# Optimization experiments

Hardware: AMD Instinct MI355X
Metric: run time of the kernel (lower is better)

## Reference

```python
import jax, jax.numpy as jnp
import numpy as np

PRIME = 2147483647  # 2^31 - 1, MinHash modulus
GAMMA = 0.3
NUM_HEADS = 8


def minhash_sketch(ids, a, b):
    # ids: (B, L, S) int64 atom ids; a,b: (K,) hash coefficients
    # h[b,l,s,k] = (a[k]*id + b[k]) mod PRIME ; signature = min over the set axis S
    h = (ids[..., None] * a + b) % PRIME          # (B, L, S, K)
    return h.min(axis=2)                          # (B, L, K)


def jaccard_from_signatures(sig_q, sig_k):
    # sig_q: (B, Lq, K), sig_k: (B, Lk, K) -> (B, Lq, Lk) fraction of matching slots.
    # Scan over the K hash slots to avoid materializing a (B,Lq,Lk,K) tensor.
    B, Lq, K = sig_q.shape
    Lk = sig_k.shape[1]

    def step(acc, cols):
        qc, kc = cols                              # (B,Lq), (B,Lk)
        return acc + (qc[:, :, None] == kc[:, None, :]).astype(jnp.float32), None

    init = jnp.zeros((B, Lq, Lk), jnp.float32)
    xs = (jnp.moveaxis(sig_q, -1, 0), jnp.moveaxis(sig_k, -1, 0))
    acc, _ = jax.lax.scan(step, init, xs)
    return acc / K


def symdiff_from_jaccard(jacc, size_q, size_k):
    # |A ∩ B| = J/(1+J) * (|A|+|B|)  =>  |A Δ B| = (|A|+|B|) * (1-J)/(1+J)
    tot = size_q[:, :, None] + size_k[:, None, :]   # (B, Lq, Lk)
    return tot * (1.0 - jacc) / (1.0 + jacc)


def setup_inputs() -> dict:
    key = jax.random.key(0)
    ks = jax.random.split(key, 12)
    B, Lq, Lk, E, S, K, V = 4, 1024, 1024, 512, 8, 128, 32000
    w = lambda k: (jax.random.normal(k, (E, E), jnp.float32) * 0.02)
    return {
        "query": jax.random.normal(ks[0], (B, Lq, E), jnp.float32),
        "key": jax.random.normal(ks[1], (B, Lk, E), jnp.float32),
        "value": jax.random.normal(ks[2], (B, Lk, E), jnp.float32),
        "token_sets_q": jax.random.randint(ks[3], (B, Lq, S), 0, V).astype(jnp.int64),
        "token_sets_k": jax.random.randint(ks[4], (B, Lk, S), 0, V).astype(jnp.int64),
        "hash_a": jax.random.randint(ks[5], (K,), 1, PRIME - 1).astype(jnp.int64),
        "hash_b": jax.random.randint(ks[6], (K,), 0, PRIME - 1).astype(jnp.int64),
        "Wq": w(ks[7]), "bq": jnp.zeros((E,), jnp.float32),
        "Wk": w(ks[8]), "bk": jnp.zeros((E,), jnp.float32),
        "Wv": w(ks[9]), "bv": jnp.zeros((E,), jnp.float32),
        "Wo": w(ks[10]), "bo": jnp.zeros((E,), jnp.float32),
    }


def reference(query, key, value, token_sets_q, token_sets_k, hash_a, hash_b,
              Wq, bq, Wk, bk, Wv, bv, Wo, bo):
    B, Lq, E = query.shape
    Lk = key.shape[1]
    H = NUM_HEADS
    d = E // H

    # in-projections (torch Linear: x @ W^T + b); q,k are computed but the
    # attention scores come solely from the token-set kernel (gating disabled)
    q = query @ Wq.T + bq
    k = key @ Wk.T + bk
    v = (value @ Wv.T + bv).reshape(B, Lk, H, d).transpose(0, 2, 1, 3)  # (B,H,Lk,d)

    # MinHash sketches of per-token atom sets -> estimated Jaccard -> Δ-RBF score
    sig_q = minhash_sketch(token_sets_q, hash_a, hash_b)   # (B,Lq,K)
    sig_k = minhash_sketch(token_sets_k, hash_a, hash_b)   # (B,Lk,K)
    jacc = jaccard_from_signatures(sig_q, sig_k)           # (B,Lq,Lk)

    S = token_sets_q.shape[-1]
    size_q = jnp.full((B, Lq), S, jnp.float32)             # uniform CSR offsets -> |set| = S
    size_k = jnp.full((B, Lk), S, jnp.float32)
    delta = symdiff_from_jaccard(jacc, size_q, size_k)
    scores = jnp.exp(-GAMMA * delta)                       # (B,Lq,Lk), shared by all heads

    attn = jax.nn.softmax(scores, axis=-1)                 # no masks, no causal, dropout=0
    ctx = jnp.einsum('bqk,bhkd->bqhd', attn, v).reshape(B, Lq, E)
    return ctx @ Wo.T + bo
```

## Files before the change

kernel.cpp:

```cpp
#include <hip/hip_runtime.h>
#include <hip/hip_bf16.h>
#include <stdint.h>

#define PRIME 2147483647u
#define GAMMA 0.3f
#define K_HASH 128
#define S_SET 8
#define NB 4
#define LQ 1024
#define LK 1024
#define EDIM 512

typedef unsigned short ushort_t;
typedef __attribute__((ext_vector_type(8))) short short8;
typedef __attribute__((ext_vector_type(4))) float f32x4;

static __device__ __forceinline__ unsigned short f2bf(float f) {
    unsigned u = __builtin_bit_cast(unsigned, f);
    u += 0x7FFFu + ((u >> 16) & 1u);
    return (unsigned short)(u >> 16);
}

static __device__ __forceinline__ void glds16(const void* g, void* l) {
    __builtin_amdgcn_global_load_lds(
        (const __attribute__((address_space(1))) unsigned int*)g,
        (__attribute__((address_space(3))) unsigned int*)l, 16, 0, 0);
}

#define SWZ(r) ((((r) >> 2) & 3) ^ ((r) & 3))

static __device__ __forceinline__ unsigned nm2(unsigned acc, unsigned a,
                                               unsigned b, unsigned ones) {
    unsigned x = a ^ b, t;
    asm("v_pk_min_u16 %0, %1, %2" : "=v"(t) : "v"(x), "v"(ones));
    return acc + t;
}
static __device__ __forceinline__ unsigned nm8(unsigned acc, int4 q, int4 k,
                                               unsigned ones) {
    acc = nm2(acc, (unsigned)q.x, (unsigned)k.x, ones);
    acc = nm2(acc, (unsigned)q.y, (unsigned)k.y, ones);
    acc = nm2(acc, (unsigned)q.z, (unsigned)k.z, ones);
    acc = nm2(acc, (unsigned)q.w, (unsigned)k.w, ones);
    return acc;
}

#define CVT_N0 (NB * LK * EDIM)
#define CVT_N1 (EDIM * EDIM)
#define CVT_N2 (EDIM * EDIM)
#define CVT_BLOCKS ((CVT_N0 + CVT_N1 + CVT_N2) / (256 * 8))
#define SIG_BLOCKS (NB * (LQ + LK) / 2)

__global__ __launch_bounds__(256) void prep_kernel(
        const float* __restrict__ v, const float* __restrict__ wv,
        const float* __restrict__ wo,
        ushort_t* __restrict__ vb, ushort_t* __restrict__ wvb,
        ushort_t* __restrict__ wob,
        const int* __restrict__ ts_q, const int* __restrict__ ts_k,
        const int* __restrict__ ha, const int* __restrict__ hb,
        ushort_t* __restrict__ sig_q, ushort_t* __restrict__ sig_k,
        float* __restrict__ rs) {
    int blk = blockIdx.x;
    if (blk < CVT_BLOCKS) {
        size_t i = ((size_t)blk * 256 + threadIdx.x) * 8;
        const float* src; ushort_t* dst; size_t off;
        if (i < CVT_N0)                { src = v;  dst = vb;  off = i; }
        else if (i < CVT_N0 + CVT_N1)  { src = wv; dst = wvb; off = i - CVT_N0; }
        else                           { src = wo; dst = wob; off = i - CVT_N0 - CVT_N1; }
        float4 a = *(const float4*)(src + off);
        float4 b = *(const float4*)(src + off + 4);
        ushort4 o0, o1;
        o0.x = f2bf(a.x); o0.y = f2bf(a.y); o0.z = f2bf(a.z); o0.w = f2bf(a.w);
        o1.x = f2bf(b.x); o1.y = f2bf(b.y); o1.z = f2bf(b.z); o1.w = f2bf(b.w);
        *(ushort4*)(dst + off)     = o0;
        *(ushort4*)(dst + off + 4) = o1;
        return;
    }
    int sb = blk - CVT_BLOCKS;
    if (sb < 16) rs[sb * 256 + threadIdx.x] = 0.f;
    int half = threadIdx.x >> 7, k = threadIdx.x & 127;
    int row = sb * 2 + half;
    const int* ts = (row < NB * LQ) ? ts_q : ts_k;
    ushort_t* sig = (row < NB * LQ) ? sig_q : sig_k;
    int idx = row & (NB * LQ - 1);
    unsigned long long a  = (unsigned)ha[k];
    unsigned long long bb = (unsigned)hb[k];
    __shared__ int ids[2][S_SET];
    if (k < S_SET) ids[half][k] = ts[idx * S_SET + k];
    __syncthreads();
    unsigned mn = 0xFFFFFFFFu;
    #pragma unroll
    for (int s = 0; s < S_SET; s++) {
        unsigned long long x = a * (unsigned long long)(unsigned)ids[half][s] + bb;
        x = (x & PRIME) + (x >> 31);
        x = (x & PRIME) + (x >> 31);
        unsigned r = (unsigned)x;
        if (r >= PRIME) r -= PRIME;
        mn = (r < mn) ? r : mn;
    }
    sig[idx * K_HASH + k] = (ushort_t)mn;
}

__global__ __launch_bounds__(256) void jaccard_kernel(
        const ushort_t* __restrict__ sig_q, const ushort_t* __restrict__ sig_k,
        ushort_t* __restrict__ P, float* __restrict__ rs) {
    __shared__ int Qs[64 * 36];
    __shared__ int Ks[64 * 36];
    __shared__ float lut[K_HASH + 1];
    int tid = threadIdx.x;
    if (tid <= K_HASH) {
        float r = (float)(K_HASH - tid) / (float)(K_HASH + tid);
        lut[tid] = expf(expf(-GAMMA * (2.0f * S_SET) * r));
    }
    int b = blockIdx.z;
    int q0 = blockIdx.y * 64, j0 = blockIdx.x * 64;
    const int4* gq = (const int4*)(sig_q + ((size_t)b * LQ + q0) * K_HASH);
    const int4* gk = (const int4*)(sig_k + ((size_t)b * LK + j0) * K_HASH);
    int tx = tid & 15, ty = tid >> 4;
    unsigned ones = 0x00010001u;
    unsigned acc[4][4] = {};
    int sr = tid >> 2, sg0 = (tid & 3) * 2;
    #pragma unroll 1
    for (int h = 0; h < 2; h++) {
        __syncthreads();
        #pragma unroll
        for (int u = 0; u < 2; u++) {
            int g = sg0 + u;
            *(int4*)&Qs[sr * 36 + ((g ^ (sr >> 2)) & 7) * 4] = gq[sr * 16 + h * 8 + g];
            *(int4*)&Ks[sr * 36 + ((g ^ (sr >> 2)) & 7) * 4] = gk[sr * 16 + h * 8 + g];
        }
        __syncthreads();
        #pragma unroll
        for (int g = 0; g < 8; g++) {
            int qx = ((g ^ ty) & 7) * 4, kx = ((g ^ tx) & 7) * 4;
            int4 qv[4], kv[4];
            #pragma unroll
            for (int i = 0; i < 4; i++)
                qv[i] = *(const int4*)&Qs[(ty * 4 + i) * 36 + qx];
            #pragma unroll
            for (int j = 0; j < 4; j++)
                kv[j] = *(const int4*)&Ks[(tx * 4 + j) * 36 + kx];
            #pragma unroll
            for (int i = 0; i < 4; i++)
                #pragma unroll
                for (int j = 0; j < 4; j++)
                    acc[i][j] = nm8(acc[i][j], qv[i], kv[j], ones);
        }
    }
    ushort_t* Pb = P + (size_t)b * LQ * LK;
    float fsum[4];
    #pragma unroll
    for (int i = 0; i < 4; i++) {
        ushort4 o;
        unsigned n0_ = (acc[i][0] & 0xFFFFu) + (acc[i][0] >> 16);
        unsigned n1_ = (acc[i][1] & 0xFFFFu) + (acc[i][1] >> 16);
        unsigned n2_ = (acc[i][2] & 0xFFFFu) + (acc[i][2] >> 16);
        unsigned n3_ = (acc[i][3] & 0xFFFFu) + (acc[i][3] >> 16);
        float p0 = lut[K_HASH - n0_], p1 = lut[K_HASH - n1_];
        float p2 = lut[K_HASH - n2_], p3 = lut[K_HASH - n3_];
        fsum[i] = (p0 + p1) + (p2 + p3);
        o.x = f2bf(p0); o.y = f2bf(p1); o.z = f2bf(p2); o.w = f2bf(p3);
        int row = q0 + ty * 4 + i;
        *(ushort4*)&Pb[(size_t)row * LK + j0 + tx * 4] = o;
    }
    __syncthreads();
    float* fs = (float*)&Qs[0];
    #pragma unroll
    for (int i = 0; i < 4; i++) fs[(ty * 4 + i) * 16 + tx] = fsum[i];
    __syncthreads();
    if (tid < 64) {
        float s = 0.f;
        #pragma unroll
        for (int t = 0; t < 16; t++) s += fs[tid * 16 + t];
        atomicAdd(&rs[(size_t)b * LQ + q0 + tid], s);
    }
}

#define EPI_ROWBIAS  0
#define EPI_ROWDIV   1
#define EPI_COLBIAS  2

template<int OUTF32, int MODE>
__global__ __launch_bounds__(256) void btgemm_kernel(
        const ushort_t* __restrict__ A, const ushort_t* __restrict__ B,
        void* __restrict__ C,
        const float* __restrict__ bias, const float* __restrict__ scale,
        int lda, int ldb, int ldc, int Kd,
        long long sA, long long sB, long long sC, long long sS) {
    __shared__ ushort_t As[2][64 * 32];
    __shared__ ushort_t Bs[2][64 * 32];
    int z = blockIdx.z;
    int m0 = blockIdx.y * 64, n0 = blockIdx.x * 64;
    int tid = threadIdx.x;
    int w = tid >> 6, lane = tid & 63;
    int wm = (w & 1) * 32, wn = (w >> 1) * 32;
    int mrow = lane & 15, kg = lane >> 4;

    int r = tid >> 2, c = (tid & 3) ^ SWZ(r);
    const ushort_t* pa = A + (size_t)z * sA + (size_t)(m0 + r) * lda + c * 8;
    const ushort_t* pb = B + (size_t)z * sB + (size_t)(n0 + r) * ldb + c * 8;

    int aoff[2], boff[2];
    #pragma unroll
    for (int s = 0; s < 2; s++) {
        int Ra = wm + s * 16 + mrow;
        aoff[s] = Ra * 32 + (kg ^ SWZ(Ra)) * 8;
        int Rb = wn + s * 16 + mrow;
        boff[s] = Rb * 32 + (kg ^ SWZ(Rb)) * 8;
    }

    f32x4 acc[2][2] = {};
    int nK = Kd >> 5;
    glds16(pa, &As[0][tid * 8]);
    glds16(pb, &Bs[0][tid * 8]);
    for (int i = 0; i < nK; i++) {
        __syncthreads();
        int cur = i & 1, nxt = cur ^ 1;
        if (i + 1 < nK) {
            int k0 = (i + 1) << 5;
            glds16(pa + k0, &As[nxt][tid * 8]);
            glds16(pb + k0, &Bs[nxt][tid * 8]);
        }
        short8 af[2], bh[2];
        #pragma unroll
        for (int s = 0; s < 2; s++) {
            af[s] = *(const short8*)&As[cur][aoff[s]];
            bh[s] = *(const short8*)&Bs[cur][boff[s]];
        }
        #pragma unroll
        for (int ii = 0; ii < 2; ii++)
            #pragma unroll
            for (int jj = 0; jj < 2; jj++)
                acc[ii][jj] = __builtin_amdgcn_mfma_f32_16x16x32_bf16(
                                  af[ii], bh[jj], acc[ii][jj], 0, 0, 0);
    }

    const float* sc = scale + (size_t)z * sS;
    int col = lane & 15, rbase = (lane >> 4) * 4;
    #pragma unroll
    for (int ii = 0; ii < 2; ii++) {
        #pragma unroll
        for (int jj = 0; jj < 2; jj++) {
            #pragma unroll
            for (int rr = 0; rr < 4; rr++) {
                int gm = m0 + wm + ii * 16 + rbase + rr;
                int gn = n0 + wn + jj * 16 + col;
                float v = acc[ii][jj][rr];
                if (MODE == EPI_ROWBIAS)     v += bias[gm];
                else if (MODE == EPI_ROWDIV) v /= sc[gm];
                else                         v += bias[gn];
                size_t cix = (size_t)z * sC + (size_t)gm * ldc + gn;
                if (OUTF32) ((float*)C)[cix] = v;
                else        ((ushort_t*)C)[cix] = f2bf(v);
            }
        }
    }
}

extern "C" void kernel_launch(void* const* d_in, const int* in_sizes, int n_in,
                              void* d_out, int out_size, void* d_ws, size_t ws_size,
                              hipStream_t stream) {
    const float* value = (const float*)d_in[2];
    const int* tsq = (const int*)d_in[3];
    const int* tsk = (const int*)d_in[4];
    const int* ha  = (const int*)d_in[5];
    const int* hb  = (const int*)d_in[6];
    const float* Wv = (const float*)d_in[11];
    const float* bv = (const float*)d_in[12];
    const float* Wo = (const float*)d_in[13];
    const float* bo = (const float*)d_in[14];
    float* out = (float*)d_out;

    char* ws = (char*)d_ws;
    ushort_t* sigq   = (ushort_t*)(ws);
    ushort_t* sigk   = (ushort_t*)(ws + (1ull << 20));
    ushort_t* P      = (ushort_t*)(ws + (4ull << 20));
    float* rs        = (float*)(ws + (12ull << 20));
    ushort_t* Vt     = (ushort_t*)(ws + (12ull << 20) + (1ull << 16));
    ushort_t* ctx    = (ushort_t*)(ws + (17ull << 20));
    ushort_t* Vb     = (ushort_t*)(ws + (21ull << 20));
    ushort_t* Wvb    = (ushort_t*)(ws + (25ull << 20));
    ushort_t* Wob    = (ushort_t*)(ws + (25ull << 20) + (512ull << 10));

    prep_kernel<<<CVT_BLOCKS + SIG_BLOCKS, 256, 0, stream>>>(
        value, Wv, Wo, Vb, Wvb, Wob, tsq, tsk, ha, hb, sigq, sigk, rs);

    jaccard_kernel<<<dim3(LK / 64, LQ / 64, NB), 256, 0, stream>>>(sigq, sigk, P, rs);

    btgemm_kernel<0, EPI_ROWBIAS><<<dim3(4096 / 64, 512 / 64, 1), 256, 0, stream>>>(
        Wvb, Vb, Vt, bv, rs ,
        EDIM, EDIM, NB * LK, EDIM, 0LL, 0LL, 0LL, 0LL);

    btgemm_kernel<0, EPI_ROWDIV><<<dim3(EDIM / 64, LQ / 64, NB), 256, 0, stream>>>(
        P, Vt, ctx, bv , rs,
        LK, NB * LK, EDIM, LK,
        (long long)LQ * LK, (long long)LK, (long long)LQ * EDIM, (long long)LQ);

    btgemm_kernel<1, EPI_COLBIAS><<<dim3(EDIM / 64, NB * LQ / 64, 1), 256, 0, stream>>>(
        ctx, Wob, out, bo, rs ,
        EDIM, EDIM, EDIM, EDIM, 0LL, 0LL, 0LL, 0LL);
}
```

Baseline: 154.8 us.

## Merge Jaccard and V-projection GEMM into one launch, enlarge Jaccard tile

Fuses the Jaccard score kernel and the V in-projection GEMM into a single launch, with odd blocks doing GEMM tiles and even blocks doing Jaccard tiles. Both share shared memory through a union. The Jaccard tile grows from 64x64 to 128x64 query-by-key, so each thread accumulates 8x4 outputs and the loaded K signatures get more reuse. The aim is to remove one launch and let the two independent stages overlap on the GPU, at the cost of more registers and shared memory per block, plus a stray no-op shared-memory write left in the load loop.

```diff
diff --git a/kernel.cpp b/kernel.cpp
--- a/kernel.cpp
+++ b/kernel.cpp
@@ -42,6 +42,83 @@
     acc = nm2(acc, (unsigned)q.z, (unsigned)k.z, ones);
     acc = nm2(acc, (unsigned)q.w, (unsigned)k.w, ones);
     return acc;
+}
+
+#define EPI_ROWBIAS  0
+#define EPI_ROWDIV   1
+#define EPI_COLBIAS  2
+
+template<int OUTF32, int MODE>
+static __device__ void gemm64_dev(
+        const ushort_t* __restrict__ A, const ushort_t* __restrict__ B,
+        void* __restrict__ C,
+        const float* __restrict__ bias, const float* __restrict__ scale,
+        int lda, int ldb, int ldc, int Kd, int m0, int n0,
+        ushort_t* AsBase, ushort_t* BsBase, int tid) {
+    ushort_t (*As)[64 * 32] = (ushort_t (*)[64 * 32])AsBase;
+    ushort_t (*Bs)[64 * 32] = (ushort_t (*)[64 * 32])BsBase;
+    int w = tid >> 6, lane = tid & 63;
+    int wm = (w & 1) * 32, wn = (w >> 1) * 32;
+    int mrow = lane & 15, kg = lane >> 4;
+
+    int r = tid >> 2, c = (tid & 3) ^ SWZ(r);
+    const ushort_t* pa = A + (size_t)(m0 + r) * lda + c * 8;
+    const ushort_t* pb = B + (size_t)(n0 + r) * ldb + c * 8;
+
+    int aoff[2], boff[2];
+    #pragma unroll
+    for (int s = 0; s < 2; s++) {
+        int Ra = wm + s * 16 + mrow;
+        aoff[s] = Ra * 32 + (kg ^ SWZ(Ra)) * 8;
+        int Rb = wn + s * 16 + mrow;
+        boff[s] = Rb * 32 + (kg ^ SWZ(Rb)) * 8;
+    }
+
+    f32x4 acc[2][2] = {};
+    int nK = Kd >> 5;
+    glds16(pa, &As[0][tid * 8]);
+    glds16(pb, &Bs[0][tid * 8]);
+    for (int i = 0; i < nK; i++) {
+        __syncthreads();
+        int cur = i & 1, nxt = cur ^ 1;
+        if (i + 1 < nK) {
+            int k0 = (i + 1) << 5;
+            glds16(pa + k0, &As[nxt][tid * 8]);
+            glds16(pb + k0, &Bs[nxt][tid * 8]);
+        }
+        short8 af[2], bh[2];
+        #pragma unroll
+        for (int s = 0; s < 2; s++) {
+            af[s] = *(const short8*)&As[cur][aoff[s]];
+            bh[s] = *(const short8*)&Bs[cur][boff[s]];
+        }
+        #pragma unroll
+        for (int ii = 0; ii < 2; ii++)
+            #pragma unroll
+            for (int jj = 0; jj < 2; jj++)
+                acc[ii][jj] = __builtin_amdgcn_mfma_f32_16x16x32_bf16(
+                                  af[ii], bh[jj], acc[ii][jj], 0, 0, 0);
+    }
+
+    int col = lane & 15, rbase = (lane >> 4) * 4;
+    #pragma unroll
+    for (int ii = 0; ii < 2; ii++) {
+        #pragma unroll
+        for (int jj = 0; jj < 2; jj++) {
+            #pragma unroll
+            for (int rr = 0; rr < 4; rr++) {
+                int gm = m0 + wm + ii * 16 + rbase + rr;
+                int gn = n0 + wn + jj * 16 + col;
+                float v = acc[ii][jj][rr];
+                if (MODE == EPI_ROWBIAS)     v += bias[gm];
+                else if (MODE == EPI_ROWDIV) v /= scale[gm];
+                else                         v += bias[gn];
+                size_t cix = (size_t)gm * ldc + gn;
+                if (OUTF32) ((float*)C)[cix] = v;
+                else        ((ushort_t*)C)[cix] = f2bf(v);
+            }
+        }
+    }
 }
 
 #define CVT_N0 (NB * LK * EDIM)
@@ -100,84 +177,109 @@
     sig[idx * K_HASH + k] = (ushort_t)mn;
 }
 
-__global__ __launch_bounds__(256) void jaccard_kernel(
+union JacSmem {
+    struct {
+        int Qs[128 * 36];
+        int Ks[64 * 36];
+        float lut[K_HASH + 1];
+    } jac;
+    struct {
+        ushort_t As[2][64 * 32];
+        ushort_t Bs[2][64 * 32];
+    } g;
+};
+
+__global__ __launch_bounds__(256) void jacg1_kernel(
         const ushort_t* __restrict__ sig_q, const ushort_t* __restrict__ sig_k,
-        ushort_t* __restrict__ P, float* __restrict__ rs) {
-    __shared__ int Qs[64 * 36];
-    __shared__ int Ks[64 * 36];
-    __shared__ float lut[K_HASH + 1];
-    int tid = threadIdx.x;
+        ushort_t* __restrict__ P, float* __restrict__ rs,
+        const ushort_t* __restrict__ Wvb, const ushort_t* __restrict__ Vb,
+        ushort_t* __restrict__ Vt, const float* __restrict__ bv) {
+    __shared__ JacSmem sm;
+    int blk = blockIdx.x, tid = threadIdx.x;
+    if (blk & 1) {
+        int t = blk >> 1;
+        gemm64_dev<0, EPI_ROWBIAS>(Wvb, Vb, Vt, bv, nullptr,
+                                   EDIM, EDIM, NB * LK, EDIM,
+                                   (t >> 6) * 64, (t & 63) * 64,
+                                   sm.g.As[0], sm.g.Bs[0], tid);
+        return;
+    }
+    int t = blk >> 1;
     if (tid <= K_HASH) {
         float r = (float)(K_HASH - tid) / (float)(K_HASH + tid);
-        lut[tid] = expf(expf(-GAMMA * (2.0f * S_SET) * r));
-    }
-    int b = blockIdx.z;
-    int q0 = blockIdx.y * 64, j0 = blockIdx.x * 64;
+        sm.jac.lut[tid] = expf(expf(-GAMMA * (2.0f * S_SET) * r));
+    }
+    int b = t >> 7;
+    int q0 = ((t >> 4) & 7) * 128, j0 = (t & 15) * 64;
     const int4* gq = (const int4*)(sig_q + ((size_t)b * LQ + q0) * K_HASH);
     const int4* gk = (const int4*)(sig_k + ((size_t)b * LK + j0) * K_HASH);
     int tx = tid & 15, ty = tid >> 4;
     unsigned ones = 0x00010001u;
-    unsigned acc[4][4] = {};
-    int sr = tid >> 2, sg0 = (tid & 3) * 2;
+    unsigned acc[8][4] = {};
+    int sra = tid >> 2, srb = 64 + sra, sg0 = (tid & 3) * 2;
     #pragma unroll 1
     for (int h = 0; h < 2; h++) {
         __syncthreads();
         #pragma unroll
         for (int u = 0; u < 2; u++) {
             int g = sg0 + u;
-            *(int4*)&Qs[sr * 36 + ((g ^ (sr >> 2)) & 7) * 4] = gq[sr * 16 + h * 8 + g];
-            *(int4*)&Ks[sr * 36 + ((g ^ (sr >> 2)) & 7) * 4] = gk[sr * 16 + h * 8 + g];
+            sm.jac.Qs[0] += 0;
+            *(int4*)&sm.jac.Qs[sra * 36 + ((g ^ (sra >> 2)) & 7) * 4]
+                = gq[sra * 16 + h * 8 + g];
+            *(int4*)&sm.jac.Qs[srb * 36 + ((g ^ (srb >> 2)) & 7) * 4]
+                = gq[srb * 16 + h * 8 + g];
+            *(int4*)&sm.jac.Ks[sra * 36 + ((g ^ (sra >> 2)) & 7) * 4]
+                = gk[sra * 16 + h * 8 + g];
         }
         __syncthreads();
         #pragma unroll
         for (int g = 0; g < 8; g++) {
-            int qx = ((g ^ ty) & 7) * 4, kx = ((g ^ tx) & 7) * 4;
-            int4 qv[4], kv[4];
-            #pragma unroll
-            for (int i = 0; i < 4; i++)
-                qv[i] = *(const int4*)&Qs[(ty * 4 + i) * 36 + qx];
-            #pragma unroll
-            for (int j = 0; j < 4; j++)
-                kv[j] = *(const int4*)&Ks[(tx * 4 + j) * 36 + kx];
-            #pragma unroll
-            for (int i = 0; i < 4; i++)
+            int4 qv[8], kv[4];
+            #pragma unroll
+            for (int i = 0; i < 8; i++) {
+                int r = ty * 8 + i;
+                qv[i] = *(const int4*)&sm.jac.Qs[r * 36 + ((g ^ (r >> 2)) & 7) * 4];
+            }
+            #pragma unroll
+            for (int j = 0; j < 4; j++) {
+                int r = tx * 4 + j;
+                kv[j] = *(const int4*)&sm.jac.Ks[r * 36 + ((g ^ (r >> 2)) & 7) * 4];
+            }
+            #pragma unroll
+            for (int i = 0; i < 8; i++)
                 #pragma unroll
                 for (int j = 0; j < 4; j++)
                     acc[i][j] = nm8(acc[i][j], qv[i], kv[j], ones);
         }
     }
     ushort_t* Pb = P + (size_t)b * LQ * LK;
-    float fsum[4];
-    #pragma unroll
-    for (int i = 0; i < 4; i++) {
+    float fsum[8];
+    #pragma unroll
+    for (int i = 0; i < 8; i++) {
         ushort4 o;
         unsigned n0_ = (acc[i][0] & 0xFFFFu) + (acc[i][0] >> 16);
         unsigned n1_ = (acc[i][1] & 0xFFFFu) + (acc[i][1] >> 16);
         unsigned n2_ = (acc[i][2] & 0xFFFFu) + (acc[i][2] >> 16);
         unsigned n3_ = (acc[i][3] & 0xFFFFu) + (acc[i][3] >> 16);
-        float p0 = lut[K_HASH - n0_], p1 = lut[K_HASH - n1_];
-        float p2 = lut[K_HASH - n2_], p3 = lut[K_HASH - n3_];
+        float p0 = sm.jac.lut[K_HASH - n0_], p1 = sm.jac.lut[K_HASH - n1_];
+        float p2 = sm.jac.lut[K_HASH - n2_], p3 = sm.jac.lut[K_HASH - n3_];
         fsum[i] = (p0 + p1) + (p2 + p3);
         o.x = f2bf(p0); o.y = f2bf(p1); o.z = f2bf(p2); o.w = f2bf(p3);
-        int row = q0 + ty * 4 + i;
+        int row = q0 + ty * 8 + i;
         *(ushort4*)&Pb[(size_t)row * LK + j0 + tx * 4] = o;
     }
     __syncthreads();
-    float* fs = (float*)&Qs[0];
-    #pragma unroll
-    for (int i = 0; i < 4; i++) fs[(ty * 4 + i) * 16 + tx] = fsum[i];
+    float* fs = (float*)&sm.jac.Qs[0];
+    #pragma unroll
+    for (int i = 0; i < 8; i++) fs[(ty * 8 + i) * 16 + tx] = fsum[i];
     __syncthreads();
-    if (tid < 64) {
+    if (tid < 128) {
         float s = 0.f;
         #pragma unroll
-        for (int t = 0; t < 16; t++) s += fs[tid * 16 + t];
+        for (int tt = 0; tt < 16; tt++) s += fs[tid * 16 + tt];
         atomicAdd(&rs[(size_t)b * LQ + q0 + tid], s);
     }
 }
-
-#define EPI_ROWBIAS  0
-#define EPI_ROWDIV   1
-#define EPI_COLBIAS  2
 
 template<int OUTF32, int MODE>
 __global__ __launch_bounds__(256) void btgemm_kernel(
@@ -186,74 +288,14 @@
         const float* __restrict__ bias, const float* __restrict__ scale,
         int lda, int ldb, int ldc, int Kd,
         long long sA, long long sB, long long sC, long long sS) {
-    __shared__ ushort_t As[2][64 * 32];
-    __shared__ ushort_t Bs[2][64 * 32];
+    __shared__ ushort_t As[2][64 * 32], Bs[2][64 * 32];
     int z = blockIdx.z;
-    int m0 = blockIdx.y * 64, n0 = blockIdx.x * 64;
-    int tid = threadIdx.x;
-    int w = tid >> 6, lane = tid & 63;
-    int wm = (w & 1) * 32, wn = (w >> 1) * 32;
-    int mrow = lane & 15, kg = lane >> 4;
-
-    int r = tid >> 2, c = (tid & 3) ^ SWZ(r);
-    const ushort_t* pa = A + (size_t)z * sA + (size_t)(m0 + r) * lda + c * 8;
-    const ushort_t* pb = B + (size_t)z * sB + (size_t)(n0 + r) * ldb + c * 8;
-
-    int aoff[2], boff[2];
-    #pragma unroll
-    for (int s = 0; s < 2; s++) {
-        int Ra = wm + s * 16 + mrow;
-        aoff[s] = Ra * 32 + (kg ^ SWZ(Ra)) * 8;
-        int Rb = wn + s * 16 + mrow;
-        boff[s] = Rb * 32 + (kg ^ SWZ(Rb)) * 8;
-    }
-
-    f32x4 acc[2][2] = {};
-    int nK = Kd >> 5;
-    glds16(pa, &As[0][tid * 8]);
-    glds16(pb, &Bs[0][tid * 8]);
-    for (int i = 0; i < nK; i++) {
-        __syncthreads();
-        int cur = i & 1, nxt = cur ^ 1;
-        if (i + 1 < nK) {
-            int k0 = (i + 1) << 5;
-            glds16(pa + k0, &As[nxt][tid * 8]);
-            glds16(pb + k0, &Bs[nxt][tid * 8]);
-        }
-        short8 af[2], bh[2];
-        #pragma unroll
-        for (int s = 0; s < 2; s++) {
-            af[s] = *(const short8*)&As[cur][aoff[s]];
-            bh[s] = *(const short8*)&Bs[cur][boff[s]];
-        }
-        #pragma unroll
-        for (int ii = 0; ii < 2; ii++)
-            #pragma unroll
-            for (int jj = 0; jj < 2; jj++)
-                acc[ii][jj] = __builtin_amdgcn_mfma_f32_16x16x32_bf16(
-                                  af[ii], bh[jj], acc[ii][jj], 0, 0, 0);
-    }
-
-    const float* sc = scale + (size_t)z * sS;
-    int col = lane & 15, rbase = (lane >> 4) * 4;
-    #pragma unroll
-    for (int ii = 0; ii < 2; ii++) {
-        #pragma unroll
-        for (int jj = 0; jj < 2; jj++) {
-            #pragma unroll
-            for (int rr = 0; rr < 4; rr++) {
-                int gm = m0 + wm + ii * 16 + rbase + rr;
-                int gn = n0 + wn + jj * 16 + col;
-                float v = acc[ii][jj][rr];
-                if (MODE == EPI_ROWBIAS)     v += bias[gm];
-                else if (MODE == EPI_ROWDIV) v /= sc[gm];
-                else                         v += bias[gn];
-                size_t cix = (size_t)z * sC + (size_t)gm * ldc + gn;
-                if (OUTF32) ((float*)C)[cix] = v;
-                else        ((ushort_t*)C)[cix] = f2bf(v);
-            }
-        }
-    }
+    gemm64_dev<OUTF32, MODE>(
+        A + (size_t)z * sA, B + (size_t)z * sB,
+        (char*)C + (size_t)z * sC * (OUTF32 ? 4 : 2),
+        bias, scale + (size_t)z * sS,
+        lda, ldb, ldc, Kd, blockIdx.y * 64, blockIdx.x * 64,
+        As[0], Bs[0], threadIdx.x);
 }
 
 extern "C" void kernel_launch(void* const* d_in, const int* in_sizes, int n_in,
@@ -284,11 +326,7 @@
     prep_kernel<<<CVT_BLOCKS + SIG_BLOCKS, 256, 0, stream>>>(
         value, Wv, Wo, Vb, Wvb, Wob, tsq, tsk, ha, hb, sigq, sigk, rs);
 
-    jaccard_kernel<<<dim3(LK / 64, LQ / 64, NB), 256, 0, stream>>>(sigq, sigk, P, rs);
-
-    btgemm_kernel<0, EPI_ROWBIAS><<<dim3(4096 / 64, 512 / 64, 1), 256, 0, stream>>>(
-        Wvb, Vb, Vt, bv, rs ,
-        EDIM, EDIM, NB * LK, EDIM, 0LL, 0LL, 0LL, 0LL);
+    jacg1_kernel<<<1024, 256, 0, stream>>>(sigq, sigk, P, rs, Wvb, Vb, Vt, bv);
 
     btgemm_kernel<0, EPI_ROWDIV><<<dim3(EDIM / 64, LQ / 64, NB), 256, 0, stream>>>(
         P, Vt, ctx, bv , rs,
```

New measurement: 173.7 us. 1.12x slower.
